# Optimization experiments

Hardware: AMD Instinct MI355X
Metric: run time of the kernel (lower is better)

## Reference

```python
import jax, jax.numpy as jnp
import numpy as np

HEADS = 20


def _sdpa(q, k, v):
    # q: [B,H,Sq,D], k/v: [B,H,Sk,D]
    scale = 1.0 / jnp.sqrt(jnp.asarray(q.shape[-1], q.dtype))
    scores = jnp.einsum('bhqd,bhkd->bhqk', q, k) * scale
    probs = jax.nn.softmax(scores, axis=-1)
    return jnp.einsum('bhqk,bhkd->bhqd', probs, v)


def _split_heads(x, B, H):
    # [B,S,H*D] -> [B,H,S,D]
    S = x.shape[1]
    D = x.shape[2] // H
    return x.reshape(B, S, H, D).transpose(0, 2, 1, 3)


def setup_inputs() -> dict:
    key = jax.random.key(0)
    ks = jax.random.split(key, 10)
    B, S, C = 4, 4096, 1280
    T, Lid, X = 77, 32, 2048
    sc = lambda fan_in: 1.0 / np.sqrt(fan_in)
    return {
        'hidden_states': jax.random.normal(ks[0], (B, S, C), jnp.float32),
        'encoder_hidden_states': jax.random.normal(ks[1], (B, T, X), jnp.float32),
        'id_embedding': jax.random.normal(ks[2], (B, Lid, X), jnp.float32),
        'Wq': jax.random.normal(ks[3], (C, C), jnp.float32) * sc(C),
        'Wk': jax.random.normal(ks[4], (C, X), jnp.float32) * sc(X),
        'Wv': jax.random.normal(ks[5], (C, X), jnp.float32) * sc(X),
        'Wik': jax.random.normal(ks[6], (C, X), jnp.float32) * sc(X),
        'Wiv': jax.random.normal(ks[7], (C, X), jnp.float32) * sc(X),
        'Wo': jax.random.normal(ks[8], (C, C), jnp.float32) * sc(C),
        'bo': jnp.zeros((C,), jnp.float32),
    }


def reference(hidden_states, encoder_hidden_states, id_embedding,
              Wq, Wk, Wv, Wik, Wiv, Wo, bo):
    id_scale = 1.0
    B, S, C = hidden_states.shape
    H = HEADS
    residual = hidden_states

    q = _split_heads(hidden_states @ Wq.T, B, H)              # [B,H,S,D]
    k = _split_heads(encoder_hidden_states @ Wk.T, B, H)      # [B,H,T,D]
    v = _split_heads(encoder_hidden_states @ Wv.T, B, H)

    cross = _sdpa(q, k, v)                                    # [B,H,S,D]

    id_k = _split_heads(id_embedding @ Wik.T, B, H)           # [B,H,Lid,D]
    id_v = _split_heads(id_embedding @ Wiv.T, B, H)
    id_out = _sdpa(q, id_k, id_v)                             # [B,H,S,D]

    combined = cross + id_scale * id_out
    combined = combined.transpose(0, 2, 1, 3).reshape(B, S, C)

    out = combined @ Wo.T + bo
    out = out + residual  # residual_connection=True, rescale_output_factor=1.0
    return out
```

## Files before the change

kernel.cpp:

```cpp
#include <hip/hip_runtime.h>

typedef short short8 __attribute__((ext_vector_type(8)));
typedef unsigned short ushort8 __attribute__((ext_vector_type(8)));
typedef float float4v __attribute__((ext_vector_type(4)));

__device__ __forceinline__ unsigned short f2bf(float f) {
    union { float f; unsigned u; } v; v.f = f;
    unsigned r = v.u + 0x7fffu + ((v.u >> 16) & 1u);
    return (unsigned short)(r >> 16);
}

__device__ __forceinline__ void async_copy16(const void* g, void* l) {
    __builtin_amdgcn_global_load_lds(
        (__attribute__((address_space(1))) void*)g,
        (__attribute__((address_space(3))) void*)l,
        16, 0, 0);
}

__global__ __launch_bounds__(256) void cast_bf16_kernel(
        const float* __restrict__ in, unsigned short* __restrict__ out, int n) {
    int i4 = (blockIdx.x * 256 + threadIdx.x) * 4;
    if (i4 < n) {
        float4 f = *(const float4*)(in + i4);
        ushort4 u;
        u.x = f2bf(f.x); u.y = f2bf(f.y); u.z = f2bf(f.z); u.w = f2bf(f.w);
        *(ushort4*)(out + i4) = u;
    }
}

__global__ __launch_bounds__(256) void cast_enc_pad_kernel(
        const float* __restrict__ in, unsigned short* __restrict__ out) {
    int i4 = blockIdx.x * 256 + threadIdx.x;
    if (i4 < 4 * 77 * 2048 / 4) {
        const int per_b = 77 * 2048 / 4;
        int b = i4 / per_b;
        int rem = i4 - b * per_b;
        float4 f = *(const float4*)(in + (size_t)i4 * 4);
        ushort4 u;
        u.x = f2bf(f.x); u.y = f2bf(f.y); u.z = f2bf(f.z); u.w = f2bf(f.w);
        *(ushort4*)(out + ((size_t)b * (96 * 2048 / 4) + rem) * 4) = u;
    }
}

struct CastBatch {
    const float* src[8];
    unsigned short* dst[8];
    int n[8];
};
__global__ __launch_bounds__(256) void cast_batch_kernel(CastBatch cb) {
    const int t = blockIdx.y;
    const int n = cb.n[t];
    int i4 = (blockIdx.x * 256 + threadIdx.x) * 4;
    if (i4 < n) {
        float4 f = *(const float4*)(cb.src[t] + i4);
        ushort4 u;
        u.x = f2bf(f.x); u.y = f2bf(f.y); u.z = f2bf(f.z); u.w = f2bf(f.w);
        *(ushort4*)(cb.dst[t] + i4) = u;
    }
}

template<int EPI>
__device__ __forceinline__ void gemm_core(
        const unsigned short* __restrict__ A,
        const unsigned short* __restrict__ B,
        float* __restrict__ Cf,
        unsigned short* __restrict__ Cb,
        const float* __restrict__ bias,
        const float* __restrict__ resid,
        int Mclamp, int N, int K, int bm, int bn) {
    __shared__ unsigned short As[128 * 64];
    __shared__ unsigned short Bs[128 * 64];

    const int tid  = threadIdx.x;
    const int lane = tid & 63;
    const int wave = tid >> 6;
    const int wm   = (wave >> 1) * 64;
    const int wn   = (wave & 1) * 64;
    const int lr   = lane & 15;
    const int lq   = lane >> 4;

    float4v acc[4][4] = {};

    const unsigned short* aptr[4];
    const unsigned short* bptr[4];
    #pragma unroll
    for (int r = 0; r < 4; ++r) {
        const int linear = r * 256 + tid;
        const int row = linear >> 3;
        const int c = (linear & 7) ^ (row & 7);
        int ar = bm + row; if (ar >= Mclamp) ar = Mclamp - 1;
        aptr[r] = A + (size_t)ar * K + c * 8;
        bptr[r] = B + (size_t)(bn + row) * K + c * 8;
    }

    for (int ks = 0; ks < K; ks += 64) {
        #pragma unroll
        for (int r = 0; r < 4; ++r) {
            async_copy16(aptr[r] + ks, (char*)As + (size_t)(r * 256 + tid) * 16);
            async_copy16(bptr[r] + ks, (char*)Bs + (size_t)(r * 256 + tid) * 16);
        }
        __syncthreads();

        #pragma unroll
        for (int kw = 0; kw < 2; ++kw) {
            short8 af[4], bfr[4];
            #pragma unroll
            for (int i = 0; i < 4; ++i) {
                const int row = wm + i * 16 + lr;
                af[i] = *(const short8*)(As + row * 64 + (((kw << 2) | lq) ^ (row & 7)) * 8);
            }
            #pragma unroll
            for (int j = 0; j < 4; ++j) {
                const int row = wn + j * 16 + lr;
                bfr[j] = *(const short8*)(Bs + row * 64 + (((kw << 2) | lq) ^ (row & 7)) * 8);
            }
            #pragma unroll
            for (int i = 0; i < 4; ++i)
                #pragma unroll
                for (int j = 0; j < 4; ++j)
                    acc[i][j] = __builtin_amdgcn_mfma_f32_16x16x32_bf16(
                                    af[i], bfr[j], acc[i][j], 0, 0, 0);
        }
        __syncthreads();
    }

    #pragma unroll
    for (int i = 0; i < 4; ++i) {
        #pragma unroll
        for (int r = 0; r < 4; ++r) {
            const int row = bm + wm + i * 16 + lq * 4 + r;
            const size_t base = (size_t)row * N;
            #pragma unroll
            for (int j = 0; j < 4; ++j) {
                const int col = bn + wn + j * 16 + lr;
                const float v = acc[i][j][r];
                const size_t idx = base + col;
                if (EPI == 2)      Cf[idx] = v + bias[col] + resid[idx];
                else if (EPI == 1) Cb[idx] = f2bf(v);
                else               Cf[idx] = v;
            }
        }
    }
}

template<int EPI>
__global__ __launch_bounds__(256) void gemm_bt_kernel(
        const unsigned short* __restrict__ A,
        const unsigned short* __restrict__ B,
        float* __restrict__ Cf,
        unsigned short* __restrict__ Cb,
        const float* __restrict__ bias,
        const float* __restrict__ resid,
        int Mclamp, int N, int K) {
    gemm_core<EPI>(A, B, Cf, Cb, bias, resid, Mclamp, N, K,
                   blockIdx.x * 128, blockIdx.y * 128);
}

__global__ __launch_bounds__(256) void gemm_kv4_kernel(
        const unsigned short* __restrict__ Aenc,
        const unsigned short* __restrict__ Aid,
        const unsigned short* __restrict__ Wk,
        const unsigned short* __restrict__ Wv,
        const unsigned short* __restrict__ Wik,
        const unsigned short* __restrict__ Wiv,
        unsigned short* __restrict__ Kb, unsigned short* __restrict__ Vb,
        unsigned short* __restrict__ IKb, unsigned short* __restrict__ IVb,
        int N, int K) {
    const int z = blockIdx.z;
    const int bm = blockIdx.x * 128;
    const int Mrows = (z < 2) ? 384 : 128;
    if (bm >= Mrows) return;
    const unsigned short* A = (z < 2) ? Aenc : Aid;
    const unsigned short* B = (z == 0) ? Wk : (z == 1) ? Wv : (z == 2) ? Wik : Wiv;
    unsigned short* C = (z == 0) ? Kb : (z == 1) ? Vb : (z == 2) ? IKb : IVb;
    gemm_core<1>(A, B, nullptr, C, nullptr, nullptr, Mrows, N, K,
                 bm, blockIdx.y * 128);
}

#define VT_STRIDE 136
__global__ __launch_bounds__(256) void attn_mfma_kernel(
        const unsigned short* __restrict__ Q,
        const unsigned short* __restrict__ Kb,
        const unsigned short* __restrict__ Vb,
        const unsigned short* __restrict__ IKb,
        const unsigned short* __restrict__ IVb,
        unsigned short* __restrict__ Cmb) {
    const int b = blockIdx.z;
    const int h = blockIdx.y;
    const int hoff = h * 64;
    const int qbase = blockIdx.x * 64;
    const int tid = threadIdx.x;
    const int lane = tid & 63;
    const int wave = tid >> 6;
    const int l15 = lane & 15;
    const int quad = lane >> 4;

    __shared__ unsigned short Vt[64 * VT_STRIDE];
    __shared__ unsigned short Pl[64 * VT_STRIDE];

    for (int i = tid; i < 96 * 8; i += 256) {
        const int c = i / 96;
        const int key = i - c * 96;
        short8 v = *(const short8*)(Vb + (size_t)(b * 96 + key) * 1280 + hoff + c * 8);
        #pragma unroll
        for (int j = 0; j < 8; ++j)
            Vt[(c * 8 + j) * VT_STRIDE + key] = (unsigned short)v[j];
    }
    {
        const int c = tid >> 5;
        const int key = tid & 31;
        short8 v = *(const short8*)(IVb + (size_t)(b * 32 + key) * 1280 + hoff + c * 8);
        #pragma unroll
        for (int j = 0; j < 8; ++j)
            Vt[(c * 8 + j) * VT_STRIDE + 96 + key] = (unsigned short)v[j];
    }
    __syncthreads();

    const int qrow = b * 4096 + qbase + wave * 16 + l15;
    const unsigned short* qp = Q + (size_t)qrow * 1280 + hoff + quad * 8;
    const short8 aQ0 = *(const short8*)(qp);
    const short8 aQ1 = *(const short8*)(qp + 32);

    const float scale = 0.125f;
    float lC[4] = {0.f, 0.f, 0.f, 0.f};
    float lI[4] = {0.f, 0.f, 0.f, 0.f};

    #pragma unroll
    for (int t = 0; t < 5; ++t) {
        const unsigned short* kp = Kb + (size_t)(b * 96 + t * 16 + l15) * 1280 + hoff + quad * 8;
        const short8 bK0 = *(const short8*)(kp);
        const short8 bK1 = *(const short8*)(kp + 32);
        float4v s = {};
        s = __builtin_amdgcn_mfma_f32_16x16x32_bf16(aQ0, bK0, s, 0, 0, 0);
        s = __builtin_amdgcn_mfma_f32_16x16x32_bf16(aQ1, bK1, s, 0, 0, 0);
        #pragma unroll
        for (int r = 0; r < 4; ++r) {
            float p = __expf(s[r] * scale);
            if (t == 4 && l15 >= 13) p = 0.f;
            lC[r] += p;
            Pl[(wave * 16 + quad * 4 + r) * VT_STRIDE + t * 16 + l15] = f2bf(p);
        }
    }
    #pragma unroll
    for (int r = 0; r < 4; ++r)
        Pl[(wave * 16 + quad * 4 + r) * VT_STRIDE + 80 + l15] = 0;

    #pragma unroll
    for (int t = 0; t < 2; ++t) {
        const unsigned short* kp = IKb + (size_t)(b * 32 + t * 16 + l15) * 1280 + hoff + quad * 8;
        const short8 bK0 = *(const short8*)(kp);
        const short8 bK1 = *(const short8*)(kp + 32);
        float4v s = {};
        s = __builtin_amdgcn_mfma_f32_16x16x32_bf16(aQ0, bK0, s, 0, 0, 0);
        s = __builtin_amdgcn_mfma_f32_16x16x32_bf16(aQ1, bK1, s, 0, 0, 0);
        #pragma unroll
        for (int r = 0; r < 4; ++r) {
            const float p = __expf(s[r] * scale);
            lI[r] += p;
            Pl[(wave * 16 + quad * 4 + r) * VT_STRIDE + 96 + t * 16 + l15] = f2bf(p);
        }
    }

    #pragma unroll
    for (int m = 1; m <= 8; m <<= 1) {
        #pragma unroll
        for (int r = 0; r < 4; ++r) {
            lC[r] += __shfl_xor(lC[r], m);
            lI[r] += __shfl_xor(lI[r], m);
        }
    }
    __syncthreads();

    float4v oC[4] = {};
    float4v oI[4] = {};
    #pragma unroll
    for (int kt = 0; kt < 3; ++kt) {
        const short8 aP = *(const short8*)(Pl + (wave * 16 + l15) * VT_STRIDE + kt * 32 + quad * 8);
        #pragma unroll
        for (int td = 0; td < 4; ++td) {
            const short8 bV = *(const short8*)(Vt + (td * 16 + l15) * VT_STRIDE + kt * 32 + quad * 8);
            oC[td] = __builtin_amdgcn_mfma_f32_16x16x32_bf16(aP, bV, oC[td], 0, 0, 0);
        }
    }
    {
        const short8 aP = *(const short8*)(Pl + (wave * 16 + l15) * VT_STRIDE + 96 + quad * 8);
        #pragma unroll
        for (int td = 0; td < 4; ++td) {
            const short8 bV = *(const short8*)(Vt + (td * 16 + l15) * VT_STRIDE + 96 + quad * 8);
            oI[td] = __builtin_amdgcn_mfma_f32_16x16x32_bf16(aP, bV, oI[td], 0, 0, 0);
        }
    }

    float rc[4], ri[4];
    #pragma unroll
    for (int r = 0; r < 4; ++r) { rc[r] = 1.f / lC[r]; ri[r] = 1.f / lI[r]; }

    #pragma unroll
    for (int td = 0; td < 4; ++td) {
        #pragma unroll
        for (int r = 0; r < 4; ++r) {
            const int row = b * 4096 + qbase + wave * 16 + quad * 4 + r;
            const int col = hoff + td * 16 + l15;
            Cmb[(size_t)row * 1280 + col] = f2bf(oC[td][r] * rc[r] + oI[td][r] * ri[r]);
        }
    }
}

extern "C" void kernel_launch(void* const* d_in, const int* in_sizes, int n_in,
                              void* d_out, int out_size, void* d_ws, size_t ws_size,
                              hipStream_t stream) {
    const float* hs  = (const float*)d_in[0];
    const float* enc = (const float*)d_in[1];
    const float* idm = (const float*)d_in[2];
    const float* Wq  = (const float*)d_in[3];
    const float* Wk  = (const float*)d_in[4];
    const float* Wv  = (const float*)d_in[5];
    const float* Wik = (const float*)d_in[6];
    const float* Wiv = (const float*)d_in[7];
    const float* Wo  = (const float*)d_in[8];
    const float* bo  = (const float*)d_in[9];
    float* out = (float*)d_out;

    char* ws = (char*)d_ws;
    size_t off = 0;
    auto carve = [&](size_t bytes) {
        char* p = ws + off;
        off += (bytes + 255) & ~(size_t)255;
        return p;
    };

    unsigned short* Xh   = (unsigned short*)carve(16384ULL * 1280 * 2);
    unsigned short* Wq_b = (unsigned short*)carve(1280ULL * 1280 * 2);
    unsigned short* Wk_b = (unsigned short*)carve(1280ULL * 2048 * 2);
    unsigned short* Wv_b = (unsigned short*)carve(1280ULL * 2048 * 2);
    unsigned short* Wik_b= (unsigned short*)carve(1280ULL * 2048 * 2);
    unsigned short* Wiv_b= (unsigned short*)carve(1280ULL * 2048 * 2);
    unsigned short* Wo_b = (unsigned short*)carve(1280ULL * 1280 * 2);
    unsigned short* Encb = (unsigned short*)carve(384ULL * 2048 * 2);
    unsigned short* Idb  = (unsigned short*)carve(128ULL * 2048 * 2);
    unsigned short* Qb   = (unsigned short*)carve(16384ULL * 1280 * 2);
    unsigned short* Kb   = (unsigned short*)carve(384ULL * 1280 * 2);
    unsigned short* Vb   = (unsigned short*)carve(384ULL * 1280 * 2);
    unsigned short* IKb  = (unsigned short*)carve(128ULL * 1280 * 2);
    unsigned short* IVb  = (unsigned short*)carve(128ULL * 1280 * 2);
    (void)ws_size; (void)in_sizes; (void)n_in; (void)out_size;

    cast_bf16_kernel<<<(4 * 4096 * 1280 / 4 + 255) / 256, 256, 0, stream>>>(
        hs, Xh, 4 * 4096 * 1280);
    cast_enc_pad_kernel<<<(4 * 77 * 2048 / 4 + 255) / 256, 256, 0, stream>>>(enc, Encb);

    CastBatch cb;
    cb.src[0] = Wq;  cb.dst[0] = Wq_b;  cb.n[0] = 1280 * 1280;
    cb.src[1] = Wk;  cb.dst[1] = Wk_b;  cb.n[1] = 1280 * 2048;
    cb.src[2] = Wv;  cb.dst[2] = Wv_b;  cb.n[2] = 1280 * 2048;
    cb.src[3] = Wik; cb.dst[3] = Wik_b; cb.n[3] = 1280 * 2048;
    cb.src[4] = Wiv; cb.dst[4] = Wiv_b; cb.n[4] = 1280 * 2048;
    cb.src[5] = Wo;  cb.dst[5] = Wo_b;  cb.n[5] = 1280 * 1280;
    cb.src[6] = idm; cb.dst[6] = Idb;   cb.n[6] = 4 * 32 * 2048;
    cb.src[7] = nullptr; cb.dst[7] = nullptr; cb.n[7] = 0;
    cast_batch_kernel<<<dim3((1280 * 2048 / 4 + 255) / 256, 7), 256, 0, stream>>>(cb);

    gemm_bt_kernel<1><<<dim3(128, 10), 256, 0, stream>>>(
        Xh, Wq_b, nullptr, Qb, nullptr, nullptr, 16384, 1280, 1280);

    gemm_kv4_kernel<<<dim3(3, 10, 4), 256, 0, stream>>>(
        Encb, Idb, Wk_b, Wv_b, Wik_b, Wiv_b, Kb, Vb, IKb, IVb, 1280, 2048);

    attn_mfma_kernel<<<dim3(64, 20, 4), 256, 0, stream>>>(Qb, Kb, Vb, IKb, IVb, Xh);

    gemm_bt_kernel<2><<<dim3(128, 10), 256, 0, stream>>>(
        Xh, Wo_b, out, nullptr, bo, hs, 16384, 1280, 1280);
}
```

Before: 477.7 us.

## Replace 128x128 GEMM with 256x256-tile 512-thread double-buffered GEMM for Q/O projections

Adds a new GEMM kernel with 256x256 output tiles, 8 waves, and double-buffered async global-to-LDS loads using an XOR-swizzled LDS layout. It splits each K step into two MFMA halves, raises wave priority around the second half, and remaps workgroup IDs across 8 groups to improve L2 locality. It is used for the Q projection and the output projection with bias/residual, replacing the 128x128 kernel. The larger tiles raise reuse per byte loaded but need 128KB of LDS and many accumulator registers, which limits occupancy. The grid also shrinks to 320 blocks, which may leave compute units unevenly loaded.

```diff
diff --git a/kernel.cpp b/kernel.cpp
--- a/kernel.cpp
+++ b/kernel.cpp
@@ -141,19 +141,6 @@
             }
         }
     }
-}
-
-template<int EPI>
-__global__ __launch_bounds__(256) void gemm_bt_kernel(
-        const unsigned short* __restrict__ A,
-        const unsigned short* __restrict__ B,
-        float* __restrict__ Cf,
-        unsigned short* __restrict__ Cb,
-        const float* __restrict__ bias,
-        const float* __restrict__ resid,
-        int Mclamp, int N, int K) {
-    gemm_core<EPI>(A, B, Cf, Cb, bias, resid, Mclamp, N, K,
-                   blockIdx.x * 128, blockIdx.y * 128);
 }
 
 __global__ __launch_bounds__(256) void gemm_kv4_kernel(
@@ -177,6 +164,132 @@
                  bm, blockIdx.y * 128);
 }
 
+template<int EPI>
+__global__ __launch_bounds__(512) void gemm256_kernel(
+        const unsigned short* __restrict__ A,
+        const unsigned short* __restrict__ B,
+        float* __restrict__ Cf,
+        unsigned short* __restrict__ Cb,
+        const float* __restrict__ bias,
+        const float* __restrict__ resid,
+        int N, int K, int tn) {
+    __shared__ unsigned short As[2][256 * 64];
+    __shared__ unsigned short Bs[2][256 * 64];
+
+    const int tid  = threadIdx.x;
+    const int lane = tid & 63;
+    const int wave = tid >> 6;
+    const int wm   = (wave >> 2) * 128;
+    const int wn   = (wave & 3) * 64;
+    const int l15  = lane & 15;
+    const int lq   = lane >> 4;
+
+    int wg = blockIdx.x;
+    const int q = gridDim.x >> 3;
+    wg = (wg & 7) * q + (wg >> 3);
+    const int mt = wg / tn;
+    const int nt = wg - mt * tn;
+    const int bm = mt * 256;
+    const int bn = nt * 256;
+
+    float4v acc[8][4] = {};
+
+    const unsigned short* aptr[4];
+    const unsigned short* bptr[4];
+    #pragma unroll
+    for (int r = 0; r < 4; ++r) {
+        const int linear = r * 512 + tid;
+        const int row = linear >> 3;
+        const int c = (linear & 7) ^ (row & 7);
+        aptr[r] = A + (size_t)(bm + row) * K + c * 8;
+        bptr[r] = B + (size_t)(bn + row) * K + c * 8;
+    }
+
+    auto stage = [&](int ks, int b) {
+        #pragma unroll
+        for (int r = 0; r < 4; ++r)
+            async_copy16(aptr[r] + ks, (char*)&As[b][0] + (r * 512 + tid) * 16);
+        #pragma unroll
+        for (int r = 0; r < 4; ++r)
+            async_copy16(bptr[r] + ks, (char*)&Bs[b][0] + (r * 512 + tid) * 16);
+    };
+
+    const int NT = K >> 6;
+    stage(0, 0);
+    stage(64, 1);
+
+    for (int t = 0; t < NT; ++t) {
+        const int cur = t & 1;
+        if (t == NT - 1) {
+            asm volatile("s_waitcnt vmcnt(0)" ::: "memory");
+        } else {
+            asm volatile("s_waitcnt vmcnt(8)" ::: "memory");
+        }
+        __builtin_amdgcn_s_barrier();
+        __builtin_amdgcn_sched_barrier(0);
+
+        short8 a0[8], b0[4], a1[8], b1[4];
+        #pragma unroll
+        for (int i = 0; i < 8; ++i) {
+            const int row = wm + i * 16 + l15;
+            a0[i] = *(const short8*)(&As[cur][row * 64 + ((lq ^ (row & 7)) << 3)]);
+        }
+        #pragma unroll
+        for (int j = 0; j < 4; ++j) {
+            const int row = wn + j * 16 + l15;
+            b0[j] = *(const short8*)(&Bs[cur][row * 64 + ((lq ^ (row & 7)) << 3)]);
+        }
+        #pragma unroll
+        for (int i = 0; i < 8; ++i)
+            #pragma unroll
+            for (int j = 0; j < 4; ++j)
+                acc[i][j] = __builtin_amdgcn_mfma_f32_16x16x32_bf16(
+                                a0[i], b0[j], acc[i][j], 0, 0, 0);
+        #pragma unroll
+        for (int i = 0; i < 8; ++i) {
+            const int row = wm + i * 16 + l15;
+            a1[i] = *(const short8*)(&As[cur][row * 64 + (((4 | lq) ^ (row & 7)) << 3)]);
+        }
+        #pragma unroll
+        for (int j = 0; j < 4; ++j) {
+            const int row = wn + j * 16 + l15;
+            b1[j] = *(const short8*)(&Bs[cur][row * 64 + (((4 | lq) ^ (row & 7)) << 3)]);
+        }
+        asm volatile("s_waitcnt lgkmcnt(0)" ::: "memory");
+        __builtin_amdgcn_sched_barrier(0);
+        if (t < NT - 2) {
+            __builtin_amdgcn_s_barrier();
+            stage((t + 2) << 6, cur);
+        }
+        __builtin_amdgcn_s_setprio(1);
+        #pragma unroll
+        for (int i = 0; i < 8; ++i)
+            #pragma unroll
+            for (int j = 0; j < 4; ++j)
+                acc[i][j] = __builtin_amdgcn_mfma_f32_16x16x32_bf16(
+                                a1[i], b1[j], acc[i][j], 0, 0, 0);
+        __builtin_amdgcn_s_setprio(0);
+    }
+
+    #pragma unroll
+    for (int i = 0; i < 8; ++i) {
+        #pragma unroll
+        for (int r = 0; r < 4; ++r) {
+            const int row = bm + wm + i * 16 + lq * 4 + r;
+            const size_t base = (size_t)row * N;
+            #pragma unroll
+            for (int j = 0; j < 4; ++j) {
+                const int col = bn + wn + j * 16 + l15;
+                const float v = acc[i][j][r];
+                const size_t idx = base + col;
+                if (EPI == 2)      Cf[idx] = v + bias[col] + resid[idx];
+                else if (EPI == 1) Cb[idx] = f2bf(v);
+                else               Cf[idx] = v;
+            }
+        }
+    }
+}
+
 #define VT_STRIDE 136
 __global__ __launch_bounds__(256) void attn_mfma_kernel(
         const unsigned short* __restrict__ Q,
@@ -360,14 +473,14 @@
     cb.src[7] = nullptr; cb.dst[7] = nullptr; cb.n[7] = 0;
     cast_batch_kernel<<<dim3((1280 * 2048 / 4 + 255) / 256, 7), 256, 0, stream>>>(cb);
 
-    gemm_bt_kernel<1><<<dim3(128, 10), 256, 0, stream>>>(
-        Xh, Wq_b, nullptr, Qb, nullptr, nullptr, 16384, 1280, 1280);
+    gemm256_kernel<1><<<dim3(64 * 5), 512, 0, stream>>>(
+        Xh, Wq_b, nullptr, Qb, nullptr, nullptr, 1280, 1280, 5);
 
     gemm_kv4_kernel<<<dim3(3, 10, 4), 256, 0, stream>>>(
         Encb, Idb, Wk_b, Wv_b, Wik_b, Wiv_b, Kb, Vb, IKb, IVb, 1280, 2048);
 
     attn_mfma_kernel<<<dim3(64, 20, 4), 256, 0, stream>>>(Qb, Kb, Vb, IKb, IVb, Xh);
 
-    gemm_bt_kernel<2><<<dim3(128, 10), 256, 0, stream>>>(
-        Xh, Wo_b, out, nullptr, bo, hs, 16384, 1280, 1280);
-}
+    gemm256_kernel<2><<<dim3(64 * 5), 512, 0, stream>>>(
+        Xh, Wo_b, out, nullptr, bo, hs, 1280, 1280, 5);
+}
```

Result: faster. 467.7 us (-2.1%).
